# Kernel tuning notes

Measured on AMD Instinct MI355X. Metric: run time of the kernel, lower is better.

The kernel has to match this reference:

```python
import math
import jax, jax.numpy as jnp
import numpy as np

B, N, L, E, D = 8, 4096, 256, 64, 128
Q4 = D // 4

def setup_inputs():
    key = jax.random.key(0)
    ks = jax.random.split(key, 24)
    s = 0.05
    return {
        "x_L": jax.random.normal(ks[0], (B, N), jnp.float32),
        "x_y_mask": (jax.random.uniform(ks[1], (B, N)) < 0.7).astype(jnp.float32),
        "y_mask_L": (jax.random.uniform(ks[2], (B, N)) < 0.3).astype(jnp.float32),
        "x_y_mark": jax.random.normal(ks[3], (B, L, 1), jnp.float32),
        "variable_indices": jax.random.randint(ks[4], (B, N), 0, E, jnp.int32),
        "time_indices": jax.random.randint(ks[5], (B, N), 0, L, jnp.int32),
        "N_OBS_MAX": N,
        "W_obs": jax.random.normal(ks[6], (2, D)) * s,
        "b_obs": jnp.zeros((D,), jnp.float32),
        "W_temp": jax.random.normal(ks[7], (1, D)) * s,
        "b_temp": jnp.zeros((D,), jnp.float32),
        "var_he_w": jax.random.normal(ks[8], (E, D), jnp.float32),
        "Wq": jax.random.normal(ks[9], (D, D)) * s,
        "bq": jnp.zeros((D,), jnp.float32),
        "Wk": jax.random.normal(ks[10], (D, D)) * s,
        "bk": jnp.zeros((D,), jnp.float32),
        "Wv": jax.random.normal(ks[11], (D, D)) * s,
        "bv": jnp.zeros((D,), jnp.float32),
        "threshold": jnp.float32(0.0),
        "merge_coef": jnp.float32(0.5),
        "Pr_w": jax.random.normal(ks[12], (3 * D, Q4)) * s,
        "Pr_b": jnp.zeros((Q4,), jnp.float32),
        "Pi_w": jax.random.normal(ks[13], (D, Q4)) * s,
        "Pi_b": jnp.zeros((Q4,), jnp.float32),
        "Pj_w": jax.random.normal(ks[14], (D, Q4)) * s,
        "Pj_b": jnp.zeros((Q4,), jnp.float32),
        "Pk_w": jax.random.normal(ks[15], (D, Q4)) * s,
        "Pk_b": jnp.zeros((Q4,), jnp.float32),
        "Qr": jnp.eye(Q4, dtype=jnp.float32) + jax.random.normal(ks[16], (Q4, Q4)) * s,
        "Qi": jax.random.normal(ks[17], (Q4, Q4)) * s,
        "Qj": jax.random.normal(ks[18], (Q4, Q4)) * s,
        "Qk": jax.random.normal(ks[19], (Q4, Q4)) * s,
        "fusion_bias": jnp.zeros((D,), jnp.float32),
    }

def reference(x_L, x_y_mask, y_mask_L, x_y_mark, variable_indices, time_indices,
              N_OBS_MAX, W_obs, b_obs, W_temp, b_temp, var_he_w,
              Wq, bq, Wk, bk, Wv, bv, threshold, merge_coef,
              Pr_w, Pr_b, Pi_w, Pi_b, Pj_w, Pj_b, Pk_w, Pk_b,
              Qr, Qi, Qj, Qk, fusion_bias):
    dt = x_L.dtype
    # --- HypergraphEncoder ---
    x2 = jnp.stack([x_L, 1.0 - x_y_mask + y_mask_L], axis=-1)          # (B,N,2)
    # temporal incidence: node n belongs to time hyperedge time_indices[n]
    t_inc = (time_indices[:, None, :] == jnp.arange(L)[None, :, None]).astype(dt)
    t_inc = t_inc * x_y_mask[:, None, :]                                # (B,L,N)
    v_inc = (jnp.arange(E)[None, :, None] == variable_indices[:, None, :]).astype(dt)
    v_inc = v_inc * x_y_mask[:, None, :]                                # (B,E,N)
    obs = jax.nn.relu(x2 @ W_obs + b_obs) * x_y_mask[..., None]         # (B,N,D)
    t_he = jnp.sin(x_y_mark @ W_temp + b_temp)                          # (B,L,D)
    v_he = jax.nn.relu(jnp.broadcast_to(var_he_w, (x_L.shape[0], E, D)))  # (B,E,D)
    # --- IrregularityAwareAttention over variable hyperedges ---
    q = v_he @ Wq + bq
    k = v_he @ Wk + bk
    v = v_he @ Wv + bv
    scores = jnp.einsum('bed,bfd->bef', q, k) / math.sqrt(D)            # (B,E,E)
    aux = jnp.einsum('ben,bfn->bef', v_inc, v_inc) / math.sqrt(v_inc.shape[-1])
    m = (aux != 0) & (scores > threshold)
    scores = jnp.where(m, (1.0 - merge_coef) * scores + merge_coef * aux, scores)
    attn = jax.nn.softmax(scores, axis=-1)
    v_he_att = jnp.einsum('bef,bfd->bed', attn, v)                      # (B,E,D)
    # --- gather hyperedge features to nodes via incidence ---
    tg = jnp.einsum('bln,bld->bnd', t_inc, t_he)                        # (B,N,D)
    vg = jnp.einsum('ben,bed->bnd', v_inc, v_he_att)                    # (B,N,D)
    # --- QuaternionStructuredFusion ---
    r = jnp.concatenate([obs, tg, vg], axis=-1) @ Pr_w + Pr_b           # (B,N,D/4)
    i = obs @ Pi_w + Pi_b
    j = tg @ Pj_w + Pj_b
    kq = vg @ Pk_w + Pk_b
    q_in = jnp.concatenate([r, i, j, kq], axis=-1)                      # (B,N,D)
    W = jnp.concatenate([
        jnp.concatenate([Qr, -Qi, -Qj, -Qk], axis=1),
        jnp.concatenate([Qi,  Qr, -Qk,  Qj], axis=1),
        jnp.concatenate([Qj,  Qk,  Qr, -Qi], axis=1),
        jnp.concatenate([Qk, -Qj,  Qi,  Qr], axis=1)], axis=0)          # (D,D)
    return q_in @ W.T + fusion_bias                                     # (B,N,D)
```

## Files before the change

kernel.cpp:

```cpp
#include <hip/hip_runtime.h>
#include <hip/hip_bf16.h>

#define B_ 8
#define N_ 4096
#define L_ 256
#define E_ 64
#define D_ 128

typedef const float* fp;
typedef __attribute__((ext_vector_type(8))) short short8;
typedef __attribute__((ext_vector_type(4))) float f32x4;

__device__ __forceinline__ short f2bf(float x) {
  __hip_bfloat16 h = __float2bfloat16(x);
  return __builtin_bit_cast(short, h);
}

__device__ __constant__ int   selT[16] = {0,1,2,3, 1,0,3,2, 2,3,0,1, 3,2,1,0};
__device__ __constant__ float sgnT[16] = {1.f,-1.f,-1.f,-1.f, 1.f,1.f,-1.f,1.f,
                                          1.f,1.f,1.f,-1.f, 1.f,-1.f,1.f,1.f};

__global__ __launch_bounds__(256) void k_setup(
    fp Pr_w, fp Pi_w, fp Pj_w, fp Pk_w,
    fp Pr_b, fp Pi_b, fp Pj_b, fp Pk_b,
    fp Qr, fp Qi, fp Qj, fp Qk, fp fusion_bias,
    fp var_he_w, fp Wq, fp bq, fp Wk, fp bk, fp Wv, fp bv,
    fp xmask, const int* vidx,
    float* ws) {
  int bid = blockIdx.x, tid = threadIdx.x;
  float* M = ws;
  float* c = ws + 49152;
  float* qkv = ws + 49280;
  float* cnt = ws + 73856;
  if (bid < 96) {
    __shared__ float qlds[4][32][33];
    {
      fp Qsrc[4] = {Qr, Qi, Qj, Qk};
      for (int lid = tid; lid < 4096; lid += 256) {
        int mat = lid >> 10, el = lid & 1023;
        qlds[mat][el >> 5][el & 31] = Qsrc[mat][el];
      }
    }
    __syncthreads();
    int m = bid >> 5, di0 = (bid & 31) * 4;
    int sub = tid >> 7, dd = tid & 127;
    int br = dd >> 5, a = dd & 31;
    const float* w0 = qlds[br][a];
    int t1 = br * 4 + m + 1;
    const float* w1 = qlds[selT[t1]][a];
    float s1 = sgnT[t1];
    fp Pm = (m == 0) ? Pi_w : (m == 1) ? Pj_w : Pk_w;
#pragma unroll
    for (int ii = 0; ii < 2; ++ii) {
      int di = di0 + ii * 2 + sub;
      const float* pr = Pr_w + (m * 128 + di) * 32;
      const float* pm = Pm + di * 32;
      float acc = 0.f;
#pragma unroll
      for (int q = 0; q < 32; ++q)
        acc += pr[q] * w0[q] + s1 * pm[q] * w1[q];
      if (m == 0) M[dd * 128 + di] = acc;
      else M[m * 16384 + di * 128 + dd] = acc;
    }
    if (bid == 0 && tid < 128) {
      float acc = fusion_bias ? fusion_bias[tid] : 0.f;
#pragma unroll
      for (int bc = 0; bc < 4; ++bc) {
        fp Pb = (bc == 0) ? Pr_b : (bc == 1) ? Pi_b : (bc == 2) ? Pj_b : Pk_b;
        int t = br * 4 + bc;
        const float* wr = qlds[selT[t]][a];
        float sg = sgnT[t];
        float part = 0.f;
#pragma unroll
        for (int q = 0; q < 32; ++q) part += Pb[q] * wr[q];
        acc += sg * part;
      }
      c[tid] = acc;
    }
  } else if (bid < 192) {
    int id = (bid - 96) * 256 + tid;
    int which = id >> 13, rem = id & 8191, e = rem >> 7, d = rem & 127;
    fp W = (which == 0) ? Wq : (which == 1) ? Wk : Wv;
    fp bb = (which == 0) ? bq : (which == 1) ? bk : bv;
    float acc = bb[d];
    for (int d2 = 0; d2 < 128; ++d2)
      acc += fmaxf(var_he_w[e * 128 + d2], 0.f) * W[d2 * 128 + d];
    qkv[id] = acc;
  } else {
    __shared__ int hc[64];
    int b = bid - 192;
    if (tid < 64) hc[tid] = 0;
    __syncthreads();
    for (int n = tid; n < N_; n += 256)
      if (xmask[b * N_ + n] != 0.f)
        atomicAdd(&hc[vidx[b * N_ + n] & 63], 1);
    __syncthreads();
    if (tid < 64) cnt[b * 64 + tid] = (float)hc[tid];
  }
}

__global__ __launch_bounds__(128) void k_mid(
    fp thr_p, fp mc_p, fp mark, fp W_temp, fp b_temp,
    float* ws) {
  __shared__ float buf[128];
  __shared__ float attn_s[64];
  const float* M1 = ws + 16384;
  const float* M2 = ws + 32768;
  const float* qkv = ws + 49280;
  const float* cnt = ws + 73856;
  float* VG = ws + 74368;
  float* TG = ws + 139904;
  int bid = blockIdx.x, t = threadIdx.x;
  if (bid < 512) {
    int b = bid >> 6, e = bid & 63;
    const float* q = qkv;
    const float* k = qkv + 8192;
    const float* v = qkv + 16384;
    int f = t & 63, h = t >> 6;
    float part = 0.f;
    for (int d = h * 64; d < h * 64 + 64; ++d)
      part += q[e * 128 + d] * k[f * 128 + d];
    buf[t] = part;
    __syncthreads();
    if (t < 64) {
      float s = (buf[t] + buf[t + 64]) * 0.08838834764831845f;
      if (t == e) {
        float aux = cnt[b * 64 + e] * (1.f / 64.f);
        float thv = thr_p ? thr_p[0] : 0.f;
        float mc = mc_p ? mc_p[0] : 0.5f;
        if (aux != 0.f && s > thv) s = (1.f - mc) * s + mc * aux;
      }
      float m = s;
      for (int o = 32; o; o >>= 1) m = fmaxf(m, __shfl_xor(m, o));
      float ex = __expf(s - m);
      float sum = ex;
      for (int o = 32; o; o >>= 1) sum += __shfl_xor(sum, o);
      attn_s[t] = ex / sum;
    }
    __syncthreads();
    float va = 0.f;
    for (int ff = 0; ff < 64; ++ff) va += attn_s[ff] * v[ff * 128 + t];
    __syncthreads();
    buf[t] = va;
    __syncthreads();
    float acc = 0.f;
    for (int di = 0; di < 128; ++di) acc += buf[di] * M2[di * 128 + t];
    VG[(b * 64 + e) * 128 + t] = acc;
  } else {
    int bl = bid - 512;
    buf[t] = sinf(mark[bl] * W_temp[t] + b_temp[t]);
    __syncthreads();
    float acc = 0.f;
    for (int di = 0; di < 128; ++di) acc += buf[di] * M1[di * 128 + t];
    TG[bl * 128 + t] = acc;
  }
}

__global__ __launch_bounds__(256, 2) void k_mainf(
    fp x_L, fp x_y_mask, fp y_mask_L, const int* vidx, const int* tidx,
    fp W_obs, fp b_obs, const float* ws, float* out) {
  __shared__ short m0f[16384];
  __shared__ float cs[128];
  const float* M0T = ws;
  const float* c = ws + 49152;
  const float* VG = ws + 74368;
  const float* TG = ws + 139904;
  int tid = threadIdx.x;
#pragma unroll
  for (int i = 0; i < 64; ++i) {
    int lid = tid + i * 256;
    int j = lid & 7, lane = (lid >> 3) & 63, ft = (lid >> 9) & 3, fn = lid >> 11;
    int k = ft * 32 + ((lane >> 4) << 3) + j;
    int dd = (fn << 4) + (lane & 15);
    m0f[lid] = f2bf(M0T[dd * 128 + k]);
  }
  if (tid < 128) cs[tid] = c[tid];
  __syncthreads();

  int w = tid >> 6, l = tid & 63;
  int nb = blockIdx.x * 64 + w * 16;
  int b = blockIdx.x >> 6;

  const short8* fr = (const short8*)m0f;
  short8 bf[8][4];
#pragma unroll
  for (int fn = 0; fn < 8; ++fn)
#pragma unroll
    for (int ft = 0; ft < 4; ++ft)
      bf[fn][ft] = fr[(fn * 4 + ft) * 64 + l];

  int nodeA = nb + (l & 15);
  float mask = x_y_mask[nodeA];
  float xa = x_L[nodeA];
  float xb = 1.f - mask + y_mask_L[nodeA];
  short8 af[4];
#pragma unroll
  for (int ft = 0; ft < 4; ++ft) {
#pragma unroll
    for (int j = 0; j < 8; ++j) {
      int col = ft * 32 + ((l >> 4) << 3) + j;
      float o = fmaxf(xa * W_obs[col] + xb * W_obs[128 + col] + b_obs[col], 0.f) * mask;
      af[ft][j] = f2bf(o);
    }
  }

  f32x4 acc[8];
#pragma unroll
  for (int fn = 0; fn < 8; ++fn) acc[fn] = (f32x4)(0.f);
#pragma unroll
  for (int fn = 0; fn < 8; ++fn)
#pragma unroll
    for (int ft = 0; ft < 4; ++ft)
      acc[fn] = __builtin_amdgcn_mfma_f32_16x16x32_bf16(af[ft], bf[fn][ft], acc[fn], 0, 0, 0);

  int colbase = l & 15;
#pragma unroll
  for (int rg = 0; rg < 4; ++rg) {
    int node = nb + ((l >> 4) << 2) + rg;
    float m2 = x_y_mask[node];
    int ti = tidx[node] & 255, vi = vidx[node] & 63;
    const float* tgr = TG + (b * 256 + ti) * 128;
    const float* vgr = VG + (b * 64 + vi) * 128;
    float* orow = out + node * 128;
#pragma unroll
    for (int fn = 0; fn < 8; ++fn) {
      int col = fn * 16 + colbase;
      orow[col] = acc[fn][rg] + cs[col] + m2 * (tgr[col] + vgr[col]);
    }
  }
}

extern "C" void kernel_launch(void* const* d_in, const int* in_sizes, int n_in,
                              void* d_out, int out_size, void* d_ws, size_t ws_size,
                              hipStream_t stream) {
  const void* P[33];
  {
    int p = 0;
    for (int i = 0; i < 33; ++i) {
      bool isopt = (i == 6 || i == 18 || i == 19);
      if (isopt) {
        if (p < n_in && in_sizes[p] == 1) P[i] = d_in[p++];
        else P[i] = nullptr;
      } else {
        P[i] = (p < n_in) ? d_in[p++] : nullptr;
      }
    }
  }
  fp x_L      = (fp)P[0];
  fp x_y_mask = (fp)P[1];
  fp y_mask_L = (fp)P[2];
  fp x_y_mark = (fp)P[3];
  const int* vidx = (const int*)P[4];
  const int* tidx = (const int*)P[5];
  fp W_obs = (fp)P[7];
  fp b_obs = (fp)P[8];
  fp W_temp = (fp)P[9];
  fp b_temp = (fp)P[10];
  fp var_he_w = (fp)P[11];
  fp Wq = (fp)P[12]; fp bq = (fp)P[13];
  fp Wk = (fp)P[14]; fp bk = (fp)P[15];
  fp Wv = (fp)P[16]; fp bv = (fp)P[17];
  fp thr = (fp)P[18]; fp mc = (fp)P[19];
  fp Pr_w = (fp)P[20]; fp Pr_b = (fp)P[21];
  fp Pi_w = (fp)P[22]; fp Pi_b = (fp)P[23];
  fp Pj_w = (fp)P[24]; fp Pj_b = (fp)P[25];
  fp Pk_w = (fp)P[26]; fp Pk_b = (fp)P[27];
  fp Qr = (fp)P[28]; fp Qi = (fp)P[29];
  fp Qj = (fp)P[30]; fp Qk = (fp)P[31];
  fp fusion_bias = (fp)P[32];

  float* ws = (float*)d_ws;

  hipLaunchKernelGGL(k_setup, dim3(200), dim3(256), 0, stream,
                     Pr_w, Pi_w, Pj_w, Pk_w, Pr_b, Pi_b, Pj_b, Pk_b,
                     Qr, Qi, Qj, Qk, fusion_bias,
                     var_he_w, Wq, bq, Wk, bk, Wv, bv,
                     x_y_mask, vidx, ws);
  hipLaunchKernelGGL(k_mid, dim3(2560), dim3(128), 0, stream,
                     thr, mc, x_y_mark, W_temp, b_temp, ws);
  hipLaunchKernelGGL(k_mainf, dim3(512), dim3(256), 0, stream,
                     x_L, x_y_mask, y_mask_L, vidx, tidx, W_obs, b_obs,
                     ws, (float*)d_out);
}
```

Before: 46.31 us.

## Precompute bf16 MFMA fragments in setup and batch temporal rows in mid kernel

The setup kernel now writes the M0 fusion matrix directly as bf16 in the MFMA B-fragment order, so the main kernel loads its B fragments straight from global memory. This drops the per-block LDS staging, conversion and barrier that every one of the 512 main blocks repeated. The temporal branch of the mid kernel now processes four time rows per block, reusing each M1 load four times and cutting the grid from 2560 to 1024 blocks. The bias vector is read into registers instead of shared memory; the cost is more global-memory fragment loads per wave in the main kernel.

```diff
diff --git a/kernel.cpp b/kernel.cpp
--- a/kernel.cpp
+++ b/kernel.cpp
@@ -19,6 +19,7 @@
 __device__ __constant__ int   selT[16] = {0,1,2,3, 1,0,3,2, 2,3,0,1, 3,2,1,0};
 __device__ __constant__ float sgnT[16] = {1.f,-1.f,-1.f,-1.f, 1.f,1.f,-1.f,1.f,
                                           1.f,1.f,1.f,-1.f, 1.f,-1.f,1.f,1.f};
+
 
 __global__ __launch_bounds__(256) void k_setup(
     fp Pr_w, fp Pi_w, fp Pj_w, fp Pk_w,
@@ -29,6 +30,7 @@
     float* ws) {
   int bid = blockIdx.x, tid = threadIdx.x;
   float* M = ws;
+  unsigned short* m0frag = (unsigned short*)ws;
   float* c = ws + 49152;
   float* qkv = ws + 49280;
   float* cnt = ws + 73856;
@@ -59,8 +61,13 @@
 #pragma unroll
       for (int q = 0; q < 32; ++q)
         acc += pr[q] * w0[q] + s1 * pm[q] * w1[q];
-      if (m == 0) M[dd * 128 + di] = acc;
-      else M[m * 16384 + di * 128 + dd] = acc;
+      if (m == 0) {
+        int fn = dd >> 4, ft = di >> 5, hi = (di >> 3) & 3, j = di & 7;
+        int l = hi * 16 + (dd & 15);
+        m0frag[((fn * 4 + ft) * 64 + l) * 8 + j] = (unsigned short)f2bf(acc);
+      } else {
+        M[m * 16384 + di * 128 + dd] = acc;
+      }
     }
     if (bid == 0 && tid < 128) {
       float acc = fusion_bias ? fusion_bias[tid] : 0.f;
@@ -102,8 +109,6 @@
 __global__ __launch_bounds__(128) void k_mid(
     fp thr_p, fp mc_p, fp mark, fp W_temp, fp b_temp,
     float* ws) {
-  __shared__ float buf[128];
-  __shared__ float attn_s[64];
   const float* M1 = ws + 16384;
   const float* M2 = ws + 32768;
   const float* qkv = ws + 49280;
@@ -112,6 +117,8 @@
   float* TG = ws + 139904;
   int bid = blockIdx.x, t = threadIdx.x;
   if (bid < 512) {
+    __shared__ float buf[128];
+    __shared__ float attn_s[64];
     int b = bid >> 6, e = bid & 63;
     const float* q = qkv;
     const float* k = qkv + 8192;
@@ -147,41 +154,39 @@
     for (int di = 0; di < 128; ++di) acc += buf[di] * M2[di * 128 + t];
     VG[(b * 64 + e) * 128 + t] = acc;
   } else {
-    int bl = bid - 512;
-    buf[t] = sinf(mark[bl] * W_temp[t] + b_temp[t]);
-    __syncthreads();
-    float acc = 0.f;
-    for (int di = 0; di < 128; ++di) acc += buf[di] * M1[di * 128 + t];
-    TG[bl * 128 + t] = acc;
+    __shared__ float tb[4][128];
+    int r0 = (bid - 512) * 4;
+#pragma unroll
+    for (int r = 0; r < 4; ++r)
+      tb[r][t] = sinf(mark[r0 + r] * W_temp[t] + b_temp[t]);
+    __syncthreads();
+    float a0 = 0.f, a1 = 0.f, a2 = 0.f, a3 = 0.f;
+    for (int di = 0; di < 128; ++di) {
+      float m1v = M1[di * 128 + t];
+      a0 += tb[0][di] * m1v;
+      a1 += tb[1][di] * m1v;
+      a2 += tb[2][di] * m1v;
+      a3 += tb[3][di] * m1v;
+    }
+    TG[(r0 + 0) * 128 + t] = a0;
+    TG[(r0 + 1) * 128 + t] = a1;
+    TG[(r0 + 2) * 128 + t] = a2;
+    TG[(r0 + 3) * 128 + t] = a3;
   }
 }
 
 __global__ __launch_bounds__(256, 2) void k_mainf(
     fp x_L, fp x_y_mask, fp y_mask_L, const int* vidx, const int* tidx,
     fp W_obs, fp b_obs, const float* ws, float* out) {
-  __shared__ short m0f[16384];
-  __shared__ float cs[128];
-  const float* M0T = ws;
+  const short8* fr = (const short8*)ws;
   const float* c = ws + 49152;
   const float* VG = ws + 74368;
   const float* TG = ws + 139904;
   int tid = threadIdx.x;
-#pragma unroll
-  for (int i = 0; i < 64; ++i) {
-    int lid = tid + i * 256;
-    int j = lid & 7, lane = (lid >> 3) & 63, ft = (lid >> 9) & 3, fn = lid >> 11;
-    int k = ft * 32 + ((lane >> 4) << 3) + j;
-    int dd = (fn << 4) + (lane & 15);
-    m0f[lid] = f2bf(M0T[dd * 128 + k]);
-  }
-  if (tid < 128) cs[tid] = c[tid];
-  __syncthreads();
-
   int w = tid >> 6, l = tid & 63;
   int nb = blockIdx.x * 64 + w * 16;
   int b = blockIdx.x >> 6;
 
-  const short8* fr = (const short8*)m0f;
   short8 bf[8][4];
 #pragma unroll
   for (int fn = 0; fn < 8; ++fn)
@@ -214,6 +219,9 @@
       acc[fn] = __builtin_amdgcn_mfma_f32_16x16x32_bf16(af[ft], bf[fn][ft], acc[fn], 0, 0, 0);
 
   int colbase = l & 15;
+  float cv[8];
+#pragma unroll
+  for (int fn = 0; fn < 8; ++fn) cv[fn] = c[fn * 16 + colbase];
 #pragma unroll
   for (int rg = 0; rg < 4; ++rg) {
     int node = nb + ((l >> 4) << 2) + rg;
@@ -225,7 +233,7 @@
 #pragma unroll
     for (int fn = 0; fn < 8; ++fn) {
       int col = fn * 16 + colbase;
-      orow[col] = acc[fn][rg] + cs[col] + m2 * (tgr[col] + vgr[col]);
+      orow[col] = acc[fn][rg] + cv[fn] + m2 * (tgr[col] + vgr[col]);
     }
   }
 }
@@ -276,7 +284,7 @@
                      Qr, Qi, Qj, Qk, fusion_bias,
                      var_he_w, Wq, bq, Wk, bk, Wv, bv,
                      x_y_mask, vidx, ws);
-  hipLaunchKernelGGL(k_mid, dim3(2560), dim3(128), 0, stream,
+  hipLaunchKernelGGL(k_mid, dim3(1024), dim3(128), 0, stream,
                      thr, mc, x_y_mark, W_temp, b_temp, ws);
   hipLaunchKernelGGL(k_mainf, dim3(512), dim3(256), 0, stream,
                      x_L, x_y_mask, y_mask_L, vidx, tidx, W_obs, b_obs,
```

New measurement: 42.87 us. -7.4%, faster.
